# Kernel tuning notes

Hardware: AMD Instinct MI355X
Metric: run time of the kernel (lower is better)

Reference implementation:

```python
import jax, jax.numpy as jnp
import numpy as np

HIDDEN = 1024
HEADS = 16
HEAD_DIM = HIDDEN // HEADS  # 64
ROPE_DIM = 64
ROPE_BASE = 10000.0
B, T = 2, 2048


def setup_inputs() -> dict:
    key = jax.random.key(0)
    k1, k2, k3, k4, k5, k6 = jax.random.split(key, 6)
    x = jax.random.normal(k1, (B, T, HIDDEN), dtype=jnp.float32)
    input_ids = jax.random.randint(k2, (B, T), 0, 32000)
    # torch Linear weights: [out_features, in_features]
    qkv_w = jax.random.normal(k3, (3 * HIDDEN, HIDDEN), dtype=jnp.float32) * (1.0 / np.sqrt(HIDDEN))
    qkv_b = jnp.zeros((3 * HIDDEN,), dtype=jnp.float32)
    out_w = jax.random.normal(k4, (HIDDEN, HIDDEN), dtype=jnp.float32) * (1.0 / np.sqrt(HIDDEN))
    out_b = jnp.zeros((HIDDEN,), dtype=jnp.float32)
    global_idx = jnp.array([0, 1, 2], dtype=jnp.int64)  # special_tokens values
    return {"x": x, "input_ids": input_ids, "qkv_w": qkv_w, "qkv_b": qkv_b,
            "out_w": out_w, "out_b": out_b, "global_idx": global_idx}


def _rope_cos_sin(t, offset=0):
    inv_freq = 1.0 / (ROPE_BASE ** (jnp.arange(0, ROPE_DIM, 2, dtype=jnp.float32) / ROPE_DIM))  # [ROPE_DIM/2]
    pos = jnp.arange(offset, offset + t, dtype=jnp.float32)
    freqs = pos[:, None] * inv_freq[None, :]  # [T, ROPE_DIM/2]
    return jnp.cos(freqs)[None, None], jnp.sin(freqs)[None, None]  # [1,1,T,ROPE_DIM/2]


def _apply_rotary(x, cos, sin):
    x_rot, x_pass = x[..., :ROPE_DIM], x[..., ROPE_DIM:]
    half = ROPE_DIM // 2
    x1, x2 = x_rot[..., :half], x_rot[..., half:]
    return jnp.concatenate([x1 * cos - x2 * sin, x1 * sin + x2 * cos, x_pass], axis=-1)


def reference(x, input_ids, qkv_w, qkv_b, out_w, out_b, global_idx):
    b, t, _ = x.shape
    qkv = x @ qkv_w.T + qkv_b  # [B,T,3*HIDDEN]
    q, k, v = jnp.split(qkv, 3, axis=-1)
    # -> [B, H, T, Dh]
    reshape = lambda z: z.reshape(b, t, HEADS, HEAD_DIM).transpose(0, 2, 1, 3)
    q, k, v = reshape(q), reshape(k), reshape(v)
    cos, sin = _rope_cos_sin(t)
    q = _apply_rotary(q, cos, sin)
    k = _apply_rotary(k, cos, sin)
    # causal + global-query mask
    causal = jnp.tril(jnp.ones((t, t), dtype=bool))[None, None]  # [1,1,T,T]
    global_mask = jnp.isin(input_ids, global_idx)  # [B,T]
    allow = causal | global_mask[:, None, :, None]  # [B,1,T,T]
    scale = jnp.sqrt(jnp.float32(HEAD_DIM))
    logits = jnp.einsum('bhqd,bhkd->bhqk', q, k) / scale
    neg = -jnp.finfo(logits.dtype).max
    logits = jnp.where(allow, logits, neg)
    attn = jax.nn.softmax(logits, axis=-1)
    out = jnp.einsum('bhqk,bhkd->bhqd', attn, v)  # [B,H,T,Dh]
    out = out.transpose(0, 2, 1, 3).reshape(b, t, HEADS * HEAD_DIM)
    return out @ out_w.T + out_b
```

## Files before the change

kernel.cpp:

```cpp
#include <hip/hip_runtime.h>
#include <hip/hip_bf16.h>
#include <math.h>

typedef __bf16 bf16;
typedef __bf16 bf16x8 __attribute__((ext_vector_type(8)));
typedef float floatx4 __attribute__((ext_vector_type(4)));

#define HIDDEN 1024
#define NHEADS 16
#define HDIM 64
#define TSEQ 2048
#define NBATCH 2
#define MTOT (NBATCH * TSEQ)

__device__ inline void glds16(bf16* lds, const bf16* g)
{
  __builtin_amdgcn_global_load_lds(
      (const __attribute__((address_space(1))) unsigned int*)g,
      (__attribute__((address_space(3))) unsigned int*)lds, 16, 0, 0);
}

__global__ __launch_bounds__(256) void cvt_f32_bf16(
    const float* __restrict__ src, bf16* __restrict__ dst, int n)
{
  const int i = (blockIdx.x * 256 + threadIdx.x) * 8;
  if (i >= n) return;
  const floatx4 u = *(const floatx4*)(src + i);
  const floatx4 v = *(const floatx4*)(src + i + 4);
  bf16x8 r;
#pragma unroll
  for (int j = 0; j < 4; j++) { r[j] = (bf16)u[j]; r[4 + j] = (bf16)v[j]; }
  *(bf16x8*)(dst + i) = r;
}

template <int MODE>
__global__ __launch_bounds__(256) void gemm_bt(
    const bf16* __restrict__ A, const bf16* __restrict__ W,
    const float* __restrict__ bias, float* __restrict__ C,
    bf16* __restrict__ Qb, bf16* __restrict__ Kb, bf16* __restrict__ Vb,
    int M, int N, int K)
{
  __shared__ bf16 As[128 * 32];
  __shared__ bf16 Bs[128 * 32];

  const int tid  = threadIdx.x;
  const int lane = tid & 63;
  const int wv   = tid >> 6;
  const int quad = lane >> 4;
  const int l16  = lane & 15;
  const int m0 = blockIdx.y * 128;
  const int n0 = blockIdx.x * 128;
  const int wm = (wv >> 1) * 64;
  const int wn = (wv & 1) * 64;

  const int srow = lane >> 2;
  const int scol = (lane & 3) * 8;

  floatx4 acc[4][4];
#pragma unroll
  for (int i = 0; i < 4; i++)
#pragma unroll
    for (int j = 0; j < 4; j++) acc[i][j] = (floatx4){0.f, 0.f, 0.f, 0.f};

  for (int k0 = 0; k0 < K; k0 += 32) {
    __syncthreads();
    const bf16* ga = A + (size_t)(m0 + wv * 32 + srow) * K + k0 + scol;
    glds16(As + (wv * 32) * 32, ga);
    glds16(As + (wv * 32 + 16) * 32, ga + (size_t)16 * K);
    const bf16* gb = W + (size_t)(n0 + wv * 32 + srow) * K + k0 + scol;
    glds16(Bs + (wv * 32) * 32, gb);
    glds16(Bs + (wv * 32 + 16) * 32, gb + (size_t)16 * K);
    __syncthreads();

    bf16x8 af[4], bfr[4];
#pragma unroll
    for (int i = 0; i < 4; i++)
      af[i] = *(const bf16x8*)(As + (wm + i * 16 + l16) * 32 + quad * 8);
#pragma unroll
    for (int j = 0; j < 4; j++)
      bfr[j] = *(const bf16x8*)(Bs + (wn + j * 16 + l16) * 32 + quad * 8);
#pragma unroll
    for (int i = 0; i < 4; i++)
#pragma unroll
      for (int j = 0; j < 4; j++)
        acc[i][j] = __builtin_amdgcn_mfma_f32_16x16x32_bf16(af[i], bfr[j], acc[i][j], 0, 0, 0);
  }

#pragma unroll
  for (int i = 0; i < 4; i++) {
    const int gmBase = m0 + wm + i * 16 + quad * 4;
#pragma unroll
    for (int j = 0; j < 4; j++) {
      const int gn = n0 + wn + j * 16 + l16;
      const float bs = bias[gn];
#pragma unroll
      for (int r = 0; r < 4; r++) {
        const int gm = gmBase + r;
        const float v = acc[i][j][r] + bs;
        if (MODE == 1) {
          C[(size_t)gm * N + gn] = v;
        } else {
          const int which = gn >> 10;
          const int rem = gn & 1023;
          const int h = rem >> 6, d = rem & 63;
          const int b = gm >> 11, t = gm & 2047;
          bf16* dst = (which == 0) ? Qb : (which == 1) ? Kb : Vb;
          dst[((size_t)(b * NHEADS + h) * TSEQ + t) * HDIM + d] = (bf16)v;
        }
      }
    }
  }
}

__global__ __launch_bounds__(256) void rope_kernel(bf16* __restrict__ Q,
                                                   bf16* __restrict__ K)
{
  const int idx = blockIdx.x * 256 + threadIdx.x;
  if (idx >= 32 * TSEQ * 32) return;
  const int i  = idx & 31;
  const int t  = (idx >> 5) & (TSEQ - 1);
  const int bh = idx >> 16;
  const float inv = powf(10000.0f, -(float)i * (1.0f / 32.0f));
  const float ang = (float)t * inv;
  float s, c;
  sincosf(ang, &s, &c);
  const size_t base = ((size_t)bh * TSEQ + t) * HDIM;
  {
    const float x1 = (float)Q[base + i], x2 = (float)Q[base + i + 32];
    Q[base + i]      = (bf16)(x1 * c - x2 * s);
    Q[base + i + 32] = (bf16)(x1 * s + x2 * c);
  }
  {
    const float x1 = (float)K[base + i], x2 = (float)K[base + i + 32];
    K[base + i]      = (bf16)(x1 * c - x2 * s);
    K[base + i + 32] = (bf16)(x1 * s + x2 * c);
  }
}

__global__ __launch_bounds__(256) void transpose_v(const bf16* __restrict__ V,
                                                   bf16* __restrict__ Vt)
{
  __shared__ bf16 tile[64][80];
  const int bh = blockIdx.y;
  const int t0 = blockIdx.x * 64;
  const bf16* src = V + ((size_t)bh * TSEQ + t0) * HDIM;
  for (int c = threadIdx.x; c < 512; c += 256) {
    const int r = c >> 3, c8 = (c & 7) * 8;
    *(bf16x8*)&tile[r][c8] = *(const bf16x8*)(src + (size_t)r * HDIM + c8);
  }
  __syncthreads();
  bf16* dst = Vt + (size_t)bh * HDIM * TSEQ + t0;
  for (int c = threadIdx.x; c < 512; c += 256) {
    const int d = c >> 3, t8 = (c & 7) * 8;
    bf16x8 vv;
#pragma unroll
    for (int j = 0; j < 8; j++) vv[j] = tile[t8 + j][d];
    *(bf16x8*)(dst + (size_t)d * TSEQ + t8) = vv;
  }
}

__device__ inline int swz(int g) { return (g & ~7) | ((g ^ (g >> 3) ^ (g >> 6)) & 7); }

__global__ __launch_bounds__(256) void attn_kernel(
    const bf16* __restrict__ Q, const bf16* __restrict__ K,
    const bf16* __restrict__ Vt, bf16* __restrict__ O,
    const int* __restrict__ ids, const int* __restrict__ gidx)
{
  __shared__ bf16 Ks[4096];
  __shared__ bf16 Vs[4096];
  __shared__ int flags[4];

  const int tid  = threadIdx.x;
  const int lane = tid & 63;
  const int wv   = tid >> 6;
  const int quad = lane >> 4;
  const int l16  = lane & 15;
  const int bh = blockIdx.y;
  const int b  = bh >> 4;
  const int h  = bh & 15;

  const bf16* Qp = Q + (size_t)bh * TSEQ * HDIM;
  const bf16* Kp = K + (size_t)bh * TSEQ * HDIM;
  const bf16* Vp = Vt + (size_t)bh * HDIM * TSEQ;

  const int rK  = tid >> 3;
  const int dcK = tid & 7;
  const int gk = ((rK >> 2) & 1) * 128 + (dcK >> 2) * 64 +
                 ((dcK & 3) * 16 + (((rK >> 3) << 2) | (rK & 3)));
  const int kd0 = swz(gk) * 8, kd1 = swz(gk + 256) * 8;
  const int dV = tid >> 3;
  const int uV = tid & 7;
  const int gv = (uV >> 2) * 256 + (dV >> 4) * 64 + ((uV & 3) * 16 + (dV & 15));
  const int vd0 = swz(gv) * 8, vd1 = swz(gv + 128) * 8;

  const int g0v = gidx[0], g1v = gidx[1], g2v = gidx[2];

#pragma unroll
  for (int ph = 0; ph < 2; ph++) {
    const int qt = ph ? (31 - (int)blockIdx.x) : (int)blockIdx.x;
    const int q0 = qt * 64 + wv * 16;

    const bf16x8 qf0 = *(const bf16x8*)(Qp + (size_t)(q0 + l16) * HDIM + quad * 8);
    const bf16x8 qf1 = *(const bf16x8*)(Qp + (size_t)(q0 + l16) * HDIM + 32 + quad * 8);

    const int myq = q0 + l16;
    const int myid = ids[b * TSEQ + myq];
    const int gl = (myid == g0v) | (myid == g1v) | (myid == g2v);
    flags[wv] = __any(gl);
    __syncthreads();
    const int anyg = flags[0] | flags[1] | flags[2] | flags[3];
    const int kmax = anyg ? TSEQ : (qt * 64 + 64);

    float lsum = 0.f;
    floatx4 o[4];
#pragma unroll
    for (int nt = 0; nt < 4; nt++) o[nt] = (floatx4){0.f, 0.f, 0.f, 0.f};

    bf16x8 kA = *(const bf16x8*)(Kp + tid * 8);
    bf16x8 kB = *(const bf16x8*)(Kp + 2048 + tid * 8);
    bf16x8 vA = *(const bf16x8*)(Vp + (size_t)dV * TSEQ + uV * 8);
    bf16x8 vB = *(const bf16x8*)(Vp + (size_t)(dV + 32) * TSEQ + uV * 8);

    for (int k0 = 0; k0 < kmax; k0 += 64) {
      __syncthreads();
      *(bf16x8*)(Ks + kd0) = kA;
      *(bf16x8*)(Ks + kd1) = kB;
      *(bf16x8*)(Vs + vd0) = vA;
      *(bf16x8*)(Vs + vd1) = vB;
      __syncthreads();

      if (k0 + 64 < kmax) {
        const bf16* kc = Kp + (size_t)(k0 + 64) * HDIM;
        kA = *(const bf16x8*)(kc + tid * 8);
        kB = *(const bf16x8*)(kc + 2048 + tid * 8);
        vA = *(const bf16x8*)(Vp + (size_t)dV * TSEQ + k0 + 64 + uV * 8);
        vB = *(const bf16x8*)(Vp + (size_t)(dV + 32) * TSEQ + k0 + 64 + uV * 8);
      }

#pragma unroll
      for (int g = 0; g < 2; g++) {
        const int kb = k0 + g * 32;
        const int rb = g * 256 + lane;
        const bf16x8 a00 = *(const bf16x8*)(Ks + swz(rb) * 8);
        const bf16x8 a01 = *(const bf16x8*)(Ks + swz(rb + 64) * 8);
        const bf16x8 a10 = *(const bf16x8*)(Ks + swz(rb + 128) * 8);
        const bf16x8 a11 = *(const bf16x8*)(Ks + swz(rb + 192) * 8);
        floatx4 s0 = (floatx4){0.f, 0.f, 0.f, 0.f};
        floatx4 s1 = (floatx4){0.f, 0.f, 0.f, 0.f};
        s0 = __builtin_amdgcn_mfma_f32_16x16x32_bf16(a00, qf0, s0, 0, 0, 0);
        s0 = __builtin_amdgcn_mfma_f32_16x16x32_bf16(a01, qf1, s0, 0, 0, 0);
        s1 = __builtin_amdgcn_mfma_f32_16x16x32_bf16(a10, qf0, s1, 0, 0, 0);
        s1 = __builtin_amdgcn_mfma_f32_16x16x32_bf16(a11, qf1, s1, 0, 0, 0);

        bf16x8 pf;
#pragma unroll
        for (int r = 0; r < 4; r++) {
          const int key0 = kb + quad * 8 + r;
          const int key1 = key0 + 4;
          const float p0 = (gl || key0 <= myq) ? __expf(s0[r] * 0.125f) : 0.f;
          const float p1 = (gl || key1 <= myq) ? __expf(s1[r] * 0.125f) : 0.f;
          lsum += p0 + p1;
          pf[r]     = (bf16)p0;
          pf[4 + r] = (bf16)p1;
        }

#pragma unroll
        for (int nt = 0; nt < 4; nt++) {
          const bf16x8 vf = *(const bf16x8*)(Vs + swz(g * 256 + nt * 64 + lane) * 8);
          o[nt] = __builtin_amdgcn_mfma_f32_16x16x32_bf16(pf, vf, o[nt], 0, 0, 0);
        }
      }
    }

    lsum += __shfl_xor(lsum, 16);
    lsum += __shfl_xor(lsum, 32);

#pragma unroll
    for (int r = 0; r < 4; r++) {
      const float inv = 1.0f / __shfl(lsum, quad * 4 + r);
      const int q = q0 + quad * 4 + r;
      const size_t rowoff = ((size_t)b * TSEQ + q) * HIDDEN + h * HDIM;
#pragma unroll
      for (int nt = 0; nt < 4; nt++)
        O[rowoff + nt * 16 + l16] = (bf16)(o[nt][r] * inv);
    }
  }
}

extern "C" void kernel_launch(void* const* d_in, const int* in_sizes, int n_in,
                              void* d_out, int out_size, void* d_ws, size_t ws_size,
                              hipStream_t stream)
{
  const float* x     = (const float*)d_in[0];
  const int*   ids   = (const int*)d_in[1];
  const float* qkv_w = (const float*)d_in[2];
  const float* qkv_b = (const float*)d_in[3];
  const float* out_w = (const float*)d_in[4];
  const float* out_b = (const float*)d_in[5];
  const int*   gidx  = (const int*)d_in[6];
  float* out = (float*)d_out;

  char* ws = (char*)d_ws;
  bf16* Q      = (bf16*)(ws);
  bf16* Kb     = (bf16*)(ws + (size_t)(8u << 20));
  bf16* V      = (bf16*)(ws + (size_t)(16u << 20));
  bf16* slot24 = (bf16*)(ws + (size_t)(24u << 20));
  bf16* xb     = slot24;
  bf16* Vt     = slot24;
  bf16* out_wb = slot24;
  bf16* qkv_wb = (bf16*)d_out;
  bf16* O      = V;

  cvt_f32_bf16<<<2048, 256, 0, stream>>>(x, xb, MTOT * HIDDEN);
  cvt_f32_bf16<<<1536, 256, 0, stream>>>(qkv_w, qkv_wb, 3 * HIDDEN * HIDDEN);
  gemm_bt<0><<<dim3(3072 / 128, MTOT / 128), 256, 0, stream>>>(
      xb, qkv_wb, qkv_b, nullptr, Q, Kb, V, MTOT, 3 * HIDDEN, HIDDEN);
  rope_kernel<<<(32 * TSEQ * 32) / 256, 256, 0, stream>>>(Q, Kb);
  transpose_v<<<dim3(TSEQ / 64, 32), 256, 0, stream>>>(V, Vt);
  attn_kernel<<<dim3(16, 32), 256, 0, stream>>>(Q, Kb, Vt, O, ids, gidx);
  cvt_f32_bf16<<<512, 256, 0, stream>>>(out_w, out_wb, HIDDEN * HIDDEN);
  gemm_bt<1><<<dim3(HIDDEN / 128, MTOT / 128), 256, 0, stream>>>(
      O, out_wb, out_b, out, nullptr, nullptr, nullptr, MTOT, HIDDEN, HIDDEN);
}
```

Before: 214.9 us.

## Fuse RoPE into QKV GEMM epilogue, merge conversions, remap attention blocks per XCD

The two input-conversion launches are merged into one prep kernel, which also builds a cos/sin table. RoPE is now applied inside the QKV GEMM epilogue using that table, and the standalone rope kernel, which re-read and re-wrote Q and K, is removed. The attention grid becomes 1D, with each XCD taking four (batch, head) pairs for better L2 locality of K/V, and the order of the two query-tile phases is swapped. The cost is extra table loads and more complex stores in the GEMM epilogue.

Result: slower. 220.3 us (+2.5%).

```diff
diff --git a/kernel.cpp b/kernel.cpp
--- a/kernel.cpp
+++ b/kernel.cpp
@@ -20,6 +20,32 @@
       (__attribute__((address_space(3))) unsigned int*)lds, 16, 0, 0);
 }
 
+__global__ __launch_bounds__(256) void prep_kernel(
+    const float* __restrict__ x, bf16* __restrict__ xb,
+    const float* __restrict__ qkv_w, bf16* __restrict__ qkv_wb,
+    float2* __restrict__ ropetab)
+{
+  const int bid = blockIdx.x;
+  if (bid < 3584) {
+    const float* src = (bid < 2048) ? x : qkv_w;
+    bf16* dst = (bid < 2048) ? xb : qkv_wb;
+    const int i = (((bid < 2048) ? bid : bid - 2048) * 256 + threadIdx.x) * 8;
+    const floatx4 u = *(const floatx4*)(src + i);
+    const floatx4 v = *(const floatx4*)(src + i + 4);
+    bf16x8 r;
+#pragma unroll
+    for (int j = 0; j < 4; j++) { r[j] = (bf16)u[j]; r[4 + j] = (bf16)v[j]; }
+    *(bf16x8*)(dst + i) = r;
+  } else {
+    const int idx = (bid - 3584) * 256 + threadIdx.x;
+    const int t = idx >> 5, ii = idx & 31;
+    const float inv = powf(10000.0f, -(float)ii * (1.0f / 32.0f));
+    float s, c;
+    sincosf((float)t * inv, &s, &c);
+    ropetab[idx] = make_float2(c, s);
+  }
+}
+
 __global__ __launch_bounds__(256) void cvt_f32_bf16(
     const float* __restrict__ src, bf16* __restrict__ dst, int n)
 {
@@ -38,7 +64,7 @@
     const bf16* __restrict__ A, const bf16* __restrict__ W,
     const float* __restrict__ bias, float* __restrict__ C,
     bf16* __restrict__ Qb, bf16* __restrict__ Kb, bf16* __restrict__ Vb,
-    int M, int N, int K)
+    const float2* __restrict__ ropetab, int M, int N, int K)
 {
   __shared__ bf16 As[128 * 32];
   __shared__ bf16 Bs[128 * 32];
@@ -86,54 +112,66 @@
         acc[i][j] = __builtin_amdgcn_mfma_f32_16x16x32_bf16(af[i], bfr[j], acc[i][j], 0, 0, 0);
   }
 
-#pragma unroll
-  for (int i = 0; i < 4; i++) {
-    const int gmBase = m0 + wm + i * 16 + quad * 4;
-#pragma unroll
-    for (int j = 0; j < 4; j++) {
-      const int gn = n0 + wn + j * 16 + l16;
-      const float bs = bias[gn];
-#pragma unroll
-      for (int r = 0; r < 4; r++) {
-        const int gm = gmBase + r;
-        const float v = acc[i][j][r] + bs;
-        if (MODE == 1) {
-          C[(size_t)gm * N + gn] = v;
-        } else {
-          const int which = gn >> 10;
+  if (MODE == 0) {
+    const int whichB = n0 >> 10;
+    if (whichB < 2) {
+      bf16* dst0 = (whichB == 0) ? Qb : Kb;
+#pragma unroll
+      for (int i = 0; i < 4; i++) {
+        const int gmBase = m0 + wm + i * 16 + quad * 4;
+#pragma unroll
+        for (int j2 = 0; j2 < 2; j2++) {
+          const int gn1 = n0 + wn + j2 * 16 + l16;
+          const int d1 = j2 * 16 + l16;
+          const int h = (gn1 & 1023) >> 6;
+          const float b1 = bias[gn1];
+          const float b2 = bias[gn1 + 32];
+#pragma unroll
+          for (int r = 0; r < 4; r++) {
+            const int gm = gmBase + r;
+            const int b_ = gm >> 11, t = gm & 2047;
+            const float2 cs = ropetab[t * 32 + d1];
+            const float v1 = acc[i][j2][r] + b1;
+            const float v2 = acc[i][j2 + 2][r] + b2;
+            bf16* p = dst0 + ((size_t)(b_ * NHEADS + h) * TSEQ + t) * HDIM;
+            p[d1]      = (bf16)(v1 * cs.x - v2 * cs.y);
+            p[d1 + 32] = (bf16)(v1 * cs.y + v2 * cs.x);
+          }
+        }
+      }
+    } else {
+#pragma unroll
+      for (int i = 0; i < 4; i++) {
+        const int gmBase = m0 + wm + i * 16 + quad * 4;
+#pragma unroll
+        for (int j = 0; j < 4; j++) {
+          const int gn = n0 + wn + j * 16 + l16;
+          const float bs = bias[gn];
           const int rem = gn & 1023;
           const int h = rem >> 6, d = rem & 63;
-          const int b = gm >> 11, t = gm & 2047;
-          bf16* dst = (which == 0) ? Qb : (which == 1) ? Kb : Vb;
-          dst[((size_t)(b * NHEADS + h) * TSEQ + t) * HDIM + d] = (bf16)v;
+#pragma unroll
+          for (int r = 0; r < 4; r++) {
+            const int gm = gmBase + r;
+            const int b_ = gm >> 11, t = gm & 2047;
+            Vb[((size_t)(b_ * NHEADS + h) * TSEQ + t) * HDIM + d] =
+                (bf16)(acc[i][j][r] + bs);
+          }
         }
       }
     }
-  }
-}
-
-__global__ __launch_bounds__(256) void rope_kernel(bf16* __restrict__ Q,
-                                                   bf16* __restrict__ K)
-{
-  const int idx = blockIdx.x * 256 + threadIdx.x;
-  if (idx >= 32 * TSEQ * 32) return;
-  const int i  = idx & 31;
-  const int t  = (idx >> 5) & (TSEQ - 1);
-  const int bh = idx >> 16;
-  const float inv = powf(10000.0f, -(float)i * (1.0f / 32.0f));
-  const float ang = (float)t * inv;
-  float s, c;
-  sincosf(ang, &s, &c);
-  const size_t base = ((size_t)bh * TSEQ + t) * HDIM;
-  {
-    const float x1 = (float)Q[base + i], x2 = (float)Q[base + i + 32];
-    Q[base + i]      = (bf16)(x1 * c - x2 * s);
-    Q[base + i + 32] = (bf16)(x1 * s + x2 * c);
-  }
-  {
-    const float x1 = (float)K[base + i], x2 = (float)K[base + i + 32];
-    K[base + i]      = (bf16)(x1 * c - x2 * s);
-    K[base + i + 32] = (bf16)(x1 * s + x2 * c);
+  } else {
+#pragma unroll
+    for (int i = 0; i < 4; i++) {
+      const int gmBase = m0 + wm + i * 16 + quad * 4;
+#pragma unroll
+      for (int j = 0; j < 4; j++) {
+        const int gn = n0 + wn + j * 16 + l16;
+        const float bs = bias[gn];
+#pragma unroll
+        for (int r = 0; r < 4; r++)
+          C[(size_t)(gmBase + r) * N + gn] = acc[i][j][r] + bs;
+      }
+    }
   }
 }
 
@@ -175,7 +213,11 @@
   const int wv   = tid >> 6;
   const int quad = lane >> 4;
   const int l16  = lane & 15;
-  const int bh = blockIdx.y;
+
+  const int xcd = blockIdx.x & 7;
+  const int j   = blockIdx.x >> 3;
+  const int bh  = xcd * 4 + (j >> 4);
+  const int p   = j & 15;
   const int b  = bh >> 4;
   const int h  = bh & 15;
 
@@ -197,7 +239,7 @@
 
 #pragma unroll
   for (int ph = 0; ph < 2; ph++) {
-    const int qt = ph ? (31 - (int)blockIdx.x) : (int)blockIdx.x;
+    const int qt = ph ? p : (31 - p);
     const int q0 = qt * 64 + wv * 16;
 
     const bf16x8 qf0 = *(const bf16x8*)(Qp + (size_t)(q0 + l16) * HDIM + quad * 8);
@@ -309,16 +351,16 @@
   bf16* Vt     = slot24;
   bf16* out_wb = slot24;
   bf16* qkv_wb = (bf16*)d_out;
+  float2* ropetab = (float2*)((char*)d_out + (size_t)(8u << 20));
   bf16* O      = V;
 
-  cvt_f32_bf16<<<2048, 256, 0, stream>>>(x, xb, MTOT * HIDDEN);
-  cvt_f32_bf16<<<1536, 256, 0, stream>>>(qkv_w, qkv_wb, 3 * HIDDEN * HIDDEN);
+  prep_kernel<<<3840, 256, 0, stream>>>(x, xb, qkv_w, qkv_wb, ropetab);
   gemm_bt<0><<<dim3(3072 / 128, MTOT / 128), 256, 0, stream>>>(
-      xb, qkv_wb, qkv_b, nullptr, Q, Kb, V, MTOT, 3 * HIDDEN, HIDDEN);
-  rope_kernel<<<(32 * TSEQ * 32) / 256, 256, 0, stream>>>(Q, Kb);
+      xb, qkv_wb, qkv_b, nullptr, Q, Kb, V, ropetab, MTOT, 3 * HIDDEN, HIDDEN);
   transpose_v<<<dim3(TSEQ / 64, 32), 256, 0, stream>>>(V, Vt);
-  attn_kernel<<<dim3(16, 32), 256, 0, stream>>>(Q, Kb, Vt, O, ids, gidx);
+  attn_kernel<<<512, 256, 0, stream>>>(Q, Kb, Vt, O, ids, gidx);
   cvt_f32_bf16<<<512, 256, 0, stream>>>(out_w, out_wb, HIDDEN * HIDDEN);
   gemm_bt<1><<<dim3(HIDDEN / 128, MTOT / 128), 256, 0, stream>>>(
-      O, out_wb, out_b, out, nullptr, nullptr, nullptr, MTOT, HIDDEN, HIDDEN);
-}
+      O, out_wb, out_b, out, nullptr, nullptr, nullptr, nullptr,
+      MTOT, HIDDEN, HIDDEN);
+}
```
